# Kernel tuning notes

Measured on AMD Instinct MI355X. Metric: run time of the kernel, lower is better.

## Reference

```python
import jax, jax.numpy as jnp
import numpy as np

VOCAB = 32000
EMB = 512
HID = 512
SEQ = 64
BSZ = 32
SENTS = 48


def setup_inputs() -> dict:
    key = jax.random.key(0)
    ks = jax.random.split(key, 8)
    N = BSZ * SENTS
    s = 1.0 / np.sqrt(HID)
    return {
        "concept": jax.random.randint(ks[0], (N, SEQ), 0, VOCAB, dtype=jnp.int32),
        "ex_segs": SENTS,
        "emb_table": jax.random.normal(ks[1], (VOCAB, EMB), jnp.float32) * 0.02,
        "W_eh": jax.random.normal(ks[2], (HID, EMB), jnp.float32) * (1.0 / np.sqrt(EMB)),
        "b_eh": jnp.zeros((HID,), jnp.float32),
        "h0": jax.random.normal(ks[3], (1, HID), jnp.float32) * s,
        "W_in": jax.random.normal(ks[4], (HID, HID), jnp.float32) * s,
        "W_out": jax.random.normal(ks[5], (HID, 2 * HID), jnp.float32) * s,
        "W_ih": jax.random.normal(ks[6], (3 * HID, HID), jnp.float32) * s,
        "W_hh": jax.random.normal(ks[7], (3 * HID, HID), jnp.float32) * s,
        "b_ih": jnp.zeros((3 * HID,), jnp.float32),
        "b_hh": jnp.zeros((3 * HID,), jnp.float32),
    }


def reference(concept, ex_segs, emb_table, W_eh, b_eh, h0, W_in, W_out, W_ih, W_hh, b_ih, b_hh):
    N, S = concept.shape
    bsz = N // ex_segs
    H = W_eh.shape[0]
    # embedding lookup + emb_2_hid (dropout is identity in eval)
    emb = emb_table[concept]                              # [N, S, E]
    lengths = jnp.maximum((concept != 0).sum(-1), 1)      # [N], min 1 like pad value
    hid = jax.nn.elu(jnp.einsum('nse,he->nsh', emb, W_eh) + b_eh)  # [N, S, H]
    # uniform ex_segs: pad_sequence == reshape
    mem = hid.reshape(bsz, ex_segs, S, H).transpose(1, 0, 2, 3)    # [sent, b, S, H]
    lens = lengths.reshape(bsz, ex_segs).T                          # [sent, b]
    pos = jnp.arange(S)

    def step(h, xs):
        m, l = xs                                   # m: [b,S,H], l: [b]
        # GlobalAttention('general'): score = (h W_in) . m
        q = h @ W_in.T
        scores = jnp.einsum('bd,bsd->bs', q, m)
        scores = jnp.where(pos[None, :] < l[:, None], scores, -jnp.inf)
        align = jax.nn.softmax(scores, axis=-1)
        c = jnp.einsum('bs,bsd->bd', align, m)
        x = jnp.tanh(jnp.concatenate([c, h], axis=-1) @ W_out.T)
        # GRUCell
        gi = x @ W_ih.T + b_ih
        gh = h @ W_hh.T + b_hh
        ir, iz, inn = jnp.split(gi, 3, axis=-1)
        hr, hz, hn = jnp.split(gh, 3, axis=-1)
        r = jax.nn.sigmoid(ir + hr)
        z = jax.nn.sigmoid(iz + hz)
        n = jnp.tanh(inn + r * hn)
        h_new = (1.0 - z) * n + z * h
        return h_new, None

    h_init = jnp.broadcast_to(h0, (bsz, H))
    h_final, _ = jax.lax.scan(step, h_init, (mem, lens))
    # uniform segments: one-hot(ex_segs-1) gather == last step's hidden state
    return h_final
```

## Files before the change

kernel.cpp:

```cpp
#include <hip/hip_runtime.h>
#include <hip/hip_bf16.h>
#include <stdint.h>


typedef __bf16 bf16_t;
typedef __bf16 bf16x8 __attribute__((ext_vector_type(8)));
typedef float  f32x4  __attribute__((ext_vector_type(4)));
typedef unsigned u32x4 __attribute__((ext_vector_type(4)));

#define MFMA16(a,b,c) __builtin_amdgcn_mfma_f32_16x16x32_bf16((a),(b),(c),0,0,0)

static constexpr int    RW     = 12;
static constexpr size_t V_RING = 0;
static constexpr size_t V_WEH  = V_RING + (size_t)RW*32*65536*2;
static constexpr size_t V_W2   = V_WEH + 524288;
static constexpr size_t V_WH   = V_W2  + 1048576;
static constexpr size_t V_WI   = V_WH  + 2097152;
static constexpr size_t V_LEN  = V_WI  + 1572864;
static constexpr size_t V_H    = V_LEN + 8192;
static constexpr size_t V_HBF  = V_H   + 65536;
static constexpr size_t V_GH   = V_HBF + 32768;
static constexpr size_t V_HW2  = V_GH  + 196608;
static constexpr size_t V_XC   = V_HW2 + 65536;
static constexpr size_t V_FLG  = V_XC  + 65536;
static constexpr size_t V_REL  = V_FLG + 4096;
static constexpr size_t V_PD   = V_REL + 64;
static constexpr size_t WS_V4  = V_PD  + 6144;

static constexpr size_t L_MEM   = 0;
static constexpr size_t L_WA    = 100663296;
static constexpr size_t L_WOUT  = L_WA + 2097152;
static constexpr size_t L_WIH   = L_WOUT + 1048576;
static constexpr size_t L_LEN   = L_WIH + 1572864;
static constexpr size_t L_H     = L_LEN + 8192;
static constexpr size_t L_HBF   = L_H + 65536;
static constexpr size_t L_Q     = L_HBF + 32768;
static constexpr size_t L_GH    = L_Q + 65536;
static constexpr size_t L_CBF   = L_GH + 196608;
static constexpr size_t L_XBF   = L_CBF + 32768;
static constexpr size_t L_BAR   = L_XBF + 32768;
static constexpr size_t WS_LEG  = L_BAR + 256;

__device__ __forceinline__ unsigned ld_a32(const void* p) {
  return __hip_atomic_load((const unsigned*)p, __ATOMIC_RELAXED, __HIP_MEMORY_SCOPE_AGENT);
}
__device__ __forceinline__ unsigned long long ld_a64(const void* p) {
  return __hip_atomic_load((const unsigned long long*)p, __ATOMIC_RELAXED, __HIP_MEMORY_SCOPE_AGENT);
}
__device__ __forceinline__ void st_a32(void* p, unsigned v) {
  __hip_atomic_store((unsigned*)p, v, __ATOMIC_RELAXED, __HIP_MEMORY_SCOPE_AGENT);
}
__device__ __forceinline__ void st_a64(void* p, unsigned long long v) {
  __hip_atomic_store((unsigned long long*)p, v, __ATOMIC_RELAXED, __HIP_MEMORY_SCOPE_AGENT);
}
__device__ __forceinline__ void ld16u(u32x4& d, const void* p) {
  asm volatile("global_load_dwordx4 %0, %1, off sc0 sc1"
               : "=v"(d) : "v"(p) : "memory");
}
__device__ __forceinline__ void ld16f(f32x4& d, const void* p) {
  asm volatile("global_load_dwordx4 %0, %1, off sc0 sc1"
               : "=v"(d) : "v"(p) : "memory");
}
__device__ __forceinline__ void st16(void* p, f32x4 d) {
  asm volatile("global_store_dwordx4 %0, %1, off sc0 sc1"
               :: "v"(p), "v"(d) : "memory");
}
__device__ __forceinline__ void vm_wait0() {
  asm volatile("s_waitcnt vmcnt(0)" ::: "memory");
  __builtin_amdgcn_sched_barrier(0);
}
__device__ __forceinline__ void vm_wait16() {
  asm volatile("s_waitcnt vmcnt(16)" ::: "memory");
  __builtin_amdgcn_sched_barrier(0);
}
__device__ __forceinline__ float lo_f(unsigned long long u) {
  return __builtin_bit_cast(float, (unsigned)(u & 0xffffffffu));
}
__device__ __forceinline__ float hi_f(unsigned long long u) {
  return __builtin_bit_cast(float, (unsigned)(u >> 32));
}
__device__ __forceinline__ unsigned long long pack_f2(float a, float b) {
  return (unsigned long long)__builtin_bit_cast(unsigned, a)
       | ((unsigned long long)__builtin_bit_cast(unsigned, b) << 32);
}
__device__ __forceinline__ float2 bf2f(unsigned u) {
  float2 r;
  unsigned lo = u << 16, hi = u & 0xffff0000u;
  r.x = __builtin_bit_cast(float, lo);
  r.y = __builtin_bit_cast(float, hi);
  return r;
}
__device__ __forceinline__ unsigned pack_bf2(float a, float b) {
  __bf16 ba = (__bf16)a, bb = (__bf16)b;
  unsigned short ua = __builtin_bit_cast(unsigned short, ba);
  unsigned short ub = __builtin_bit_cast(unsigned short, bb);
  return (unsigned)ua | ((unsigned)ub << 16);
}
__device__ __forceinline__ bf16x8 cvt8(float4 lo, float4 hi) {
  bf16x8 v;
  v[0]=(__bf16)lo.x; v[1]=(__bf16)lo.y; v[2]=(__bf16)lo.z; v[3]=(__bf16)lo.w;
  v[4]=(__bf16)hi.x; v[5]=(__bf16)hi.y; v[6]=(__bf16)hi.z; v[7]=(__bf16)hi.w;
  return v;
}
__device__ __forceinline__ float fsig(float x) {
  return __builtin_amdgcn_rcpf(1.f + __expf(-x));
}
__device__ __forceinline__ float ftanh(float x) {
  float e = __expf(-2.f * fabsf(x));
  float t = (1.f - e) * __builtin_amdgcn_rcpf(1.f + e);
  return __builtin_copysignf(t, x);
}
__device__ __forceinline__ void gbar(unsigned* cnt, int target) {
  __syncthreads();
  if (threadIdx.x == 0) {
    __hip_atomic_fetch_add(cnt, 1u, __ATOMIC_RELAXED, __HIP_MEMORY_SCOPE_AGENT);
    while ((int)__hip_atomic_load(cnt, __ATOMIC_RELAXED, __HIP_MEMORY_SCOPE_AGENT) < target) {
      __builtin_amdgcn_s_sleep(1);
    }
  }
  __syncthreads();
}
__device__ __forceinline__ void cbar(unsigned* flags, unsigned* rel, int myb, int phase) {
  vm_wait0();
  __syncthreads();
  if (threadIdx.x < 64) {
    if (threadIdx.x == 0)
      st_a32(flags + myb, (unsigned)phase);
    const unsigned* fp = flags + threadIdx.x;
    for (;;) {
      int v = (int)ld_a32(fp);
      if (__all(v >= phase)) break;
      __builtin_amdgcn_s_sleep(2);
    }
    if (myb == 0 && threadIdx.x == 0)
      st_a32(rel, (unsigned)phase);
  }
  __syncthreads();
}

#define LDS_AT(base, row, kb) ((base) + (size_t)(row)*1024 + ((kb) ^ (((row) & 7) << 4)))

__global__ __launch_bounds__(256) void h_init(
    const float* __restrict__ h0, float* __restrict__ h, bf16_t* __restrict__ hbf)
{
  int idx = blockIdx.x * 256 + threadIdx.x;
  float v = h0[idx & 511];
  h[idx] = v;
  hbf[idx] = (__bf16)v;
}

__global__ __launch_bounds__(256) void lengths_kernel(
    const int* __restrict__ cpt, int* __restrict__ len)
{
  int r = blockIdx.x * 256 + threadIdx.x;
  if (r < 1536) {
    int c = 0;
    for (int s = 0; s < 64; ++s) c += (cpt[r*64 + s] != 0);
    len[r] = c > 1 ? c : 1;
  }
}

__global__ __launch_bounds__(256) void prep_v4(
    const float* __restrict__ Weh, const float* __restrict__ Win,
    const float* __restrict__ Wout, const float* __restrict__ Whh,
    const float* __restrict__ Wih,
    bf16_t* __restrict__ WehB, bf16_t* __restrict__ W2,
    bf16_t* __restrict__ WH, bf16_t* __restrict__ WI)
{
  int idx = blockIdx.x * 256 + threadIdx.x;
  if (idx < 262144) {
    WehB[idx] = (__bf16)Weh[idx];
  } else if (idx < 786432) {
    int t = idx - 262144;
    int r = t >> 9, d = t & 511;
    float v = (r < 512) ? Win[(size_t)d*512 + r] : Wout[(size_t)(r-512)*1024 + d];
    W2[t] = (__bf16)v;
  } else if (idx < 1835008) {
    int t = idx - 786432;
    int r = t >> 9, d = t & 511;
    float v = (r < 1536) ? Whh[(size_t)r*512 + d] : Wout[(size_t)(r-1536)*1024 + 512 + d];
    WH[t] = (__bf16)v;
  } else if (idx < 2621440) {
    int t = idx - 1835008;
    WI[t] = (__bf16)Wih[t];
  }
}

__global__ __launch_bounds__(256, 1) void fused_scan(
    const int* __restrict__ cpt, const float* __restrict__ table,
    const float* __restrict__ beh, const int* __restrict__ lengths,
    const bf16_t* __restrict__ WehB, const bf16_t* __restrict__ W2,
    const bf16_t* __restrict__ WH, const bf16_t* __restrict__ WI,
    const float* __restrict__ b_ih, const float* __restrict__ b_hh,
    const float* __restrict__ h0,
    bf16_t* __restrict__ ring,
    float* __restrict__ ght, float* __restrict__ hW2t, float* __restrict__ xct,
    float* __restrict__ h, bf16_t* __restrict__ hbf,
    unsigned* __restrict__ flags, unsigned* __restrict__ rel,
    unsigned* __restrict__ pd, float* __restrict__ out)
{
  __shared__ __align__(16) unsigned char smem[131072];

  const int tid = threadIdx.x, lane = tid & 63, w = tid >> 6;
  const int quad = lane >> 4, l15 = lane & 15;

  if (blockIdx.x >= 64) {
    unsigned char* A1 = smem;
    unsigned char* ME = smem + 65536;
    const int pid = blockIdx.x - 64;
    for (int c = pid; c < 1536; c += 192) {
      const int i = c >> 5, g = c & 31;
      if (i >= RW) {
        const int need = 2*(i - RW) + 1;
        if (tid == 0) {
          while ((int)ld_a32(rel) < need) __builtin_amdgcn_s_sleep(4);
        }
        __syncthreads();
      }
      {
        const int nrow = g*48 + i;
        const int s = tid >> 2, q = tid & 3;
        const int tok = cpt[nrow*64 + s];
        const float* tr = table + (size_t)tok*512 + q*128;
        #pragma unroll
        for (int it = 0; it < 16; ++it) {
          float4 lo = *(const float4*)(tr + it*8);
          float4 hi = *(const float4*)(tr + it*8 + 4);
          const int kb = q*256 + it*16;
          *(bf16x8*)LDS_AT(A1, s, kb) = cvt8(lo, hi);
        }
      }
      __syncthreads();
      for (int nb = 0; nb < 8; ++nb) {
        const int n0 = w*128 + nb*16;
        const bf16_t* brow = WehB + (size_t)(n0 + l15)*512;
        f32x4 ac0={0,0,0,0}, ac1={0,0,0,0}, ac2={0,0,0,0}, ac3={0,0,0,0};
        #pragma unroll
        for (int kt = 0; kt < 16; ++kt) {
          const int k = kt*32 + quad*8, k2 = k*2;
          bf16x8 bfr = *(const bf16x8*)(brow + k);
          bf16x8 x0 = *(const bf16x8*)LDS_AT(A1, l15,      k2);
          bf16x8 x1 = *(const bf16x8*)LDS_AT(A1, 16 + l15, k2);
          bf16x8 x2 = *(const bf16x8*)LDS_AT(A1, 32 + l15, k2);
          bf16x8 x3 = *(const bf16x8*)LDS_AT(A1, 48 + l15, k2);
          ac0 = MFMA16(x0, bfr, ac0);
          ac1 = MFMA16(x1, bfr, ac1);
          ac2 = MFMA16(x2, bfr, ac2);
          ac3 = MFMA16(x3, bfr, ac3);
        }
        const float bias = beh[n0 + l15];
        f32x4 av[4] = {ac0, ac1, ac2, ac3};
        #pragma unroll
        for (int mt = 0; mt < 4; ++mt) {
          #pragma unroll
          for (int r = 0; r < 4; ++r) {
            const int m = mt*16 + quad*4 + r;
            float v = av[mt][r] + bias;
            v = v > 0.f ? v : expm1f(v);
            float v2 = __shfl_xor(v, 1);
            if ((l15 & 1) == 0) {
              const int kb = (n0 + l15)*2;
              *(unsigned*)LDS_AT(ME, m, kb) = pack_bf2(v, v2);
            }
          }
        }
      }
      __syncthreads();
      {
        bf16_t* rc = ring + ((size_t)((i % RW)*32 + g))*65536;
        for (int nb = 0; nb < 16; ++nb) {
          const int n0 = w*256 + nb*16;
          const bf16_t* brow = W2 + (size_t)(n0 + l15)*512;
          f32x4 ac0={0,0,0,0}, ac1={0,0,0,0}, ac2={0,0,0,0}, ac3={0,0,0,0};
          #pragma unroll
          for (int kt = 0; kt < 16; ++kt) {
            const int k = kt*32 + quad*8, k2 = k*2;
            bf16x8 bfr = *(const bf16x8*)(brow + k);
            bf16x8 x0 = *(const bf16x8*)LDS_AT(ME, l15,      k2);
            bf16x8 x1 = *(const bf16x8*)LDS_AT(ME, 16 + l15, k2);
            bf16x8 x2 = *(const bf16x8*)LDS_AT(ME, 32 + l15, k2);
            bf16x8 x3 = *(const bf16x8*)LDS_AT(ME, 48 + l15, k2);
            ac0 = MFMA16(x0, bfr, ac0);
            ac1 = MFMA16(x1, bfr, ac1);
            ac2 = MFMA16(x2, bfr, ac2);
            ac3 = MFMA16(x3, bfr, ac3);
          }
          f32x4 av[4] = {ac0, ac1, ac2, ac3};
          if (w < 2) {
            #pragma unroll
            for (int mt = 0; mt < 4; ++mt) {
              #pragma unroll
              for (int r = 0; r < 4; ++r) {
                const int m = mt*16 + quad*4 + r;
                float v = av[mt][r];
                float v2 = __shfl_xor(v, 1);
                if ((l15 & 1) == 0)
                  st_a32(rc + (size_t)m*512 + n0 + l15, pack_bf2(v, v2));
              }
            }
          } else {
            const int d = n0 + l15 - 512;
            #pragma unroll
            for (int mt = 0; mt < 4; ++mt) {
              #pragma unroll
              for (int r = 0; r < 4; r += 2) {
                const int m0 = mt*16 + quad*4 + r;
                st_a32(rc + 32768 + (size_t)d*64 + m0,
                       pack_bf2(av[mt][r], av[mt][r+1]));
              }
            }
          }
        }
      }
      __syncthreads();
      if (tid == 0)
        __hip_atomic_store(pd + c, 1u, __ATOMIC_RELEASE, __HIP_MEMORY_SCOPE_AGENT);
    }
    return;
  }

  unsigned short* x_lds = (unsigned short*)smem;
  float* hsm    = (float*)(smem + 16640);
  float* sc_lds = (float*)(smem + 18688);
  float* al_lds = (float*)(smem + 18944);
  float* gi_lds = (float*)(smem + 19200);

  const int g = blockIdx.x;
  const int p2 = g >> 3, q2 = g & 7;
  const int b_loc = tid >> 6, dl = tid & 63;
  const int bg = 4*p2 + b_loc, Dg = 64*q2 + dl;
  float hreg = h0[Dg];
  int phase = 0;

  for (int i = 0; i < 48; ++i) {
    if (g < 32) {
      if (tid == 0) {
        while (ld_a32(pd + (i*32 + g)) == 0u) __builtin_amdgcn_s_sleep(2);
      }
      { int t2 = tid * 2;
        unsigned long long v = ld_a64(h + g*512 + t2);
        hsm[t2] = lo_f(v); hsm[t2+1] = hi_f(v); }
      __syncthreads();
      const char* ringc = (const char*)(ring + ((size_t)((i % RW)*32 + g))*65536);
      const int s = tid >> 2, p = tid & 3;
      u32x4 pb[16], qb[16];
      {
        const char* pbase = ringc + s*1024 + p*256;
        #pragma unroll
        for (int it = 0; it < 16; ++it) ld16u(pb[it], pbase + it*16);
        const char* qbase = ringc + 65536 + (size_t)(tid*2)*128;
        #pragma unroll
        for (int it = 0; it < 16; ++it) ld16u(qb[it], qbase + it*16);
      }
      vm_wait16();
      {
        const float* qp = hsm + p*128;
        float sum = 0.f;
        #pragma unroll
        for (int it = 0; it < 16; ++it) {
          u32x4 u = pb[it];
          float2 f0 = bf2f(u[0]), f1 = bf2f(u[1]), f2 = bf2f(u[2]), f3 = bf2f(u[3]);
          const float* qq = qp + it*8;
          sum += f0.x*qq[0] + f0.y*qq[1] + f1.x*qq[2] + f1.y*qq[3]
               + f2.x*qq[4] + f2.y*qq[5] + f3.x*qq[6] + f3.y*qq[7];
        }
        sum += __shfl_xor(sum, 1);
        sum += __shfl_xor(sum, 2);
        if (p == 0) {
          int len = lengths[g*48 + i];
          sc_lds[s] = (s < len) ? sum : -1e30f;
        }
      }
      __syncthreads();
      if (tid < 64) {
        float v = sc_lds[tid];
        float mx = v;
        #pragma unroll
        for (int o = 32; o; o >>= 1) mx = fmaxf(mx, __shfl_xor(mx, o));
        float e = __expf(v - mx);
        float sm = e;
        #pragma unroll
        for (int o = 32; o; o >>= 1) sm += __shfl_xor(sm, o);
        al_lds[tid] = e * __builtin_amdgcn_rcpf(sm);
      }
      __syncthreads();
      vm_wait0();
      {
        const int d0 = tid * 2;
        float c0 = 0.f, c1 = 0.f;
        #pragma unroll
        for (int it = 0; it < 8; ++it) {
          u32x4 u = qb[it];
          const int s0 = it*8;
          float2 a0 = bf2f(u[0]), a1 = bf2f(u[1]), a2 = bf2f(u[2]), a3 = bf2f(u[3]);
          c0 += al_lds[s0]*a0.x + al_lds[s0+1]*a0.y + al_lds[s0+2]*a1.x + al_lds[s0+3]*a1.y
              + al_lds[s0+4]*a2.x + al_lds[s0+5]*a2.y + al_lds[s0+6]*a3.x + al_lds[s0+7]*a3.y;
        }
        #pragma unroll
        for (int it = 0; it < 8; ++it) {
          u32x4 u = qb[8+it];
          const int s0 = it*8;
          float2 a0 = bf2f(u[0]), a1 = bf2f(u[1]), a2 = bf2f(u[2]), a3 = bf2f(u[3]);
          c1 += al_lds[s0]*a0.x + al_lds[s0+1]*a0.y + al_lds[s0+2]*a1.x + al_lds[s0+3]*a1.y
              + al_lds[s0+4]*a2.x + al_lds[s0+5]*a2.y + al_lds[s0+6]*a3.x + al_lds[s0+7]*a3.y;
        }
        st_a32(xct + (size_t)d0*32 + g,     __builtin_bit_cast(unsigned, c0));
        st_a32(xct + (size_t)(d0+1)*32 + g, __builtin_bit_cast(unsigned, c1));
      }
    } else {
      const int q3 = g - 32, pg = q3 >> 3, qg = q3 & 7;
      const int R0 = 256*qg;
      {
        const int r = tid >> 5, c32 = tid & 31;
        const char* src = (const char*)(hbf + (size_t)(8*pg + r)*512) + c32*32;
        u32x4 a, b2;
        ld16u(a, src); ld16u(b2, src + 16);
        vm_wait0();
        char* dst = (char*)x_lds + r*1040 + c32*32;
        *(u32x4*)dst = a; *(u32x4*)(dst + 16) = b2;
      }
      __syncthreads();
      f32x4 acc[4];
      #pragma unroll
      for (int t = 0; t < 4; ++t) acc[t] = (f32x4){0,0,0,0};
      const int Rw = R0 + 64*w;
      #pragma unroll
      for (int kt = 0; kt < 16; ++kt) {
        const int k = kt*32 + quad*8;
        bf16x8 a0 = *(const bf16x8*)((char*)x_lds + l15*1040 + k*2);
        #pragma unroll
        for (int nt = 0; nt < 4; ++nt) {
          bf16x8 bfr = *(const bf16x8*)(WH + (size_t)(Rw + nt*16 + l15)*512 + k);
          acc[nt] = MFMA16(a0, bfr, acc[nt]);
        }
      }
      if (quad < 2) {
        #pragma unroll
        for (int nt = 0; nt < 4; ++nt) {
          const int R = Rw + nt*16 + l15;
          if (R < 1536) {
            const float bias = b_hh[R];
            f32x4 vals = {acc[nt][0]+bias, acc[nt][1]+bias, acc[nt][2]+bias, acc[nt][3]+bias};
            st16(ght + (size_t)R*32 + 8*pg + quad*4, vals);
          } else {
            st16(hW2t + (size_t)(R - 1536)*32 + 8*pg + quad*4, acc[nt]);
          }
        }
      }
    }
    cbar(flags, rel, g, ++phase);

    {
      const int c = tid * 2;
      f32x4 xa, xb2, ha, hb2;
      ld16f(xa,  xct  + (size_t)c*32 + 4*p2);
      ld16f(ha,  hW2t + (size_t)c*32 + 4*p2);
      ld16f(xb2, xct  + (size_t)(c+1)*32 + 4*p2);
      ld16f(hb2, hW2t + (size_t)(c+1)*32 + 4*p2);
      vm_wait0();
      #pragma unroll
      for (int r = 0; r < 4; ++r) {
        float x0 = ftanh(xa[r] + ha[r]);
        float x1 = ftanh(xb2[r] + hb2[r]);
        *(unsigned*)((char*)x_lds + r*1040 + c*2) = pack_bf2(x0, x1);
      }
    }
    __syncthreads();
    {
      const bf16_t* wp[3];
      #pragma unroll
      for (int nt = 0; nt < 3; ++nt) {
        const int lr = w*48 + nt*16 + l15;
        wp[nt] = WI + ((size_t)((lr >> 6)*512 + 64*q2 + (lr & 63)))*512;
      }
      f32x4 ga[3];
      #pragma unroll
      for (int t = 0; t < 3; ++t) ga[t] = (f32x4){0,0,0,0};
      #pragma unroll
      for (int kt = 0; kt < 16; ++kt) {
        const int k = kt*32 + quad*8;
        bf16x8 a0 = *(const bf16x8*)((char*)x_lds + l15*1040 + k*2);
        #pragma unroll
        for (int nt = 0; nt < 3; ++nt) {
          bf16x8 bfr = *(const bf16x8*)(wp[nt] + k);
          ga[nt] = MFMA16(a0, bfr, ga[nt]);
        }
      }
      if (quad == 0) {
        #pragma unroll
        for (int nt = 0; nt < 3; ++nt) {
          const int lr = w*48 + nt*16 + l15;
          #pragma unroll
          for (int r = 0; r < 4; ++r) gi_lds[lr*4 + r] = ga[nt][r];
        }
      }
    }
    __syncthreads();
    {
      float ir = gi_lds[dl*4 + b_loc]        + b_ih[Dg];
      float iz = gi_lds[(64+dl)*4 + b_loc]   + b_ih[512 + Dg];
      float in = gi_lds[(128+dl)*4 + b_loc]  + b_ih[1024 + Dg];
      float hr = __builtin_bit_cast(float, ld_a32(ght + (size_t)Dg*32 + bg));
      float hz = __builtin_bit_cast(float, ld_a32(ght + (size_t)(512 + Dg)*32 + bg));
      float hn = __builtin_bit_cast(float, ld_a32(ght + (size_t)(1024 + Dg)*32 + bg));
      float rr = fsig(ir + hr);
      float zz = fsig(iz + hz);
      float nn = ftanh(in + rr * hn);
      float res = (1.f - zz) * nn + zz * hreg;
      hreg = res;
      if (i == 47) {
        out[bg*512 + Dg] = res;
      } else {
        float o2 = __shfl_xor(res, 1);
        if ((dl & 1) == 0) {
          st_a64(h + bg*512 + Dg, pack_f2(res, o2));
          st_a32(hbf + bg*512 + Dg, pack_bf2(res, o2));
        }
      }
    }
    if (i == 47) break;
    cbar(flags, rel, g, ++phase);
  }
}

__global__ __launch_bounds__(256) void prep_legacy(
    const float* __restrict__ Win, const float* __restrict__ Whh,
    const float* __restrict__ Wout, const float* __restrict__ Wih,
    bf16_t* __restrict__ WA, bf16_t* __restrict__ WoutB, bf16_t* __restrict__ WihB)
{
  int idx = blockIdx.x * 256 + threadIdx.x;
  if (idx < 262144)        WA[idx]            = (__bf16)Win[idx];
  else if (idx < 1048576)  WA[idx]            = (__bf16)Whh[idx - 262144];
  else if (idx < 1572864)  WoutB[idx-1048576] = (__bf16)Wout[idx - 1048576];
  else if (idx < 2359296)  WihB[idx-1572864]  = (__bf16)Wih[idx - 1572864];
}

__global__ __launch_bounds__(256) void embed_gemm(
    const int* __restrict__ cpt, const float* __restrict__ table,
    const float* __restrict__ Weh, const float* __restrict__ beh,
    bf16_t* __restrict__ mem)
{
  __shared__ unsigned short A_lds[64][40];
  __shared__ unsigned short B_lds[64][40];
  const int bid = blockIdx.x;
  const int M0 = (bid >> 3) * 64;
  const int N0 = (bid & 7) * 64;
  const int tid = threadIdx.x, lane = tid & 63, w = tid >> 6;
  const int l15 = lane & 15, quad = lane >> 4;
  const int srow = tid >> 2;
  const int koff = (tid & 3) * 8;
  const int tok = cpt[M0 + srow];
  const float* arow = table + (size_t)tok * 512;
  const float* brow = Weh + (size_t)(N0 + srow) * 512;

  f32x4 acc0 = {0,0,0,0}, acc1 = {0,0,0,0}, acc2 = {0,0,0,0}, acc3 = {0,0,0,0};
  for (int kt = 0; kt < 16; ++kt) {
    const int k0 = kt * 32;
    float4 alo = *(const float4*)(arow + k0 + koff);
    float4 ahi = *(const float4*)(arow + k0 + koff + 4);
    float4 blo = *(const float4*)(brow + k0 + koff);
    float4 bhi = *(const float4*)(brow + k0 + koff + 4);
    __syncthreads();
    *(bf16x8*)(&A_lds[srow][koff]) = cvt8(alo, ahi);
    *(bf16x8*)(&B_lds[srow][koff]) = cvt8(blo, bhi);
    __syncthreads();
    const int kq = quad * 8;
    bf16x8 bfr = *(const bf16x8*)(&B_lds[16*w + l15][kq]);
    bf16x8 a0 = *(const bf16x8*)(&A_lds[l15][kq]);
    bf16x8 a1 = *(const bf16x8*)(&A_lds[16 + l15][kq]);
    bf16x8 a2 = *(const bf16x8*)(&A_lds[32 + l15][kq]);
    bf16x8 a3 = *(const bf16x8*)(&A_lds[48 + l15][kq]);
    acc0 = MFMA16(a0, bfr, acc0);
    acc1 = MFMA16(a1, bfr, acc1);
    acc2 = MFMA16(a2, bfr, acc2);
    acc3 = MFMA16(a3, bfr, acc3);
  }
  const int n = N0 + 16*w + l15;
  const float bias = beh[n];
  f32x4 accs[4] = {acc0, acc1, acc2, acc3};
  #pragma unroll
  for (int mt = 0; mt < 4; ++mt) {
    #pragma unroll
    for (int r = 0; r < 4; ++r) {
      int m = M0 + mt*16 + quad*4 + r;
      float v = accs[mt][r] + bias;
      v = v > 0.f ? v : expm1f(v);
      int s = m & 63, nrow = m >> 6;
      int sent = nrow % 48, b = nrow / 48;
      mem[(((size_t)(sent*32 + b))*64 + s)*512 + n] = (__bf16)v;
    }
  }
}

__global__ __launch_bounds__(256) void scan_legacy(
    const bf16_t* __restrict__ mem, const int* __restrict__ lengths,
    const bf16_t* __restrict__ WA, const bf16_t* __restrict__ Wout, const bf16_t* __restrict__ Wih,
    const float* __restrict__ b_ih, const float* __restrict__ b_hh,
    float* __restrict__ q, float* __restrict__ gh,
    float* __restrict__ h, bf16_t* __restrict__ hbf,
    bf16_t* __restrict__ cbf, bf16_t* __restrict__ xbf,
    unsigned* __restrict__ bar, float* __restrict__ out)
{
  __shared__ __align__(16) unsigned char smem[52352];
  unsigned short* h_lds = (unsigned short*)smem;
  unsigned short* x_lds = (unsigned short*)smem;
  float* q_lds  = (float*)(smem + 33280);
  float* sc_lds = (float*)(smem + 35328);
  float* al_lds = (float*)(smem + 35584);
  unsigned short* c_lds = (unsigned short*)(smem + 33280);
  float* xb_lds = (float*)(smem + 50176);
  float* gi_lds = (float*)(smem + 33280);

  const int g = blockIdx.x, tid = threadIdx.x, lane = tid & 63, w = tid >> 6;
  const int quad = lane >> 4, l15 = lane & 15;
  int phase = 0;

  for (int i = 0; i < 48; ++i) {
    for (int it = 0; it < 16; ++it) {
      int chunk = tid + 256*it;
      int row = chunk >> 7, cc = chunk & 127;
      unsigned long long v = ld_a64(hbf + row*512 + cc*4);
      *(unsigned long long*)((char*)h_lds + row*1040 + cc*8) = v;
    }
    __syncthreads();
    {
      f32x4 acc0 = {0,0,0,0}, acc1 = {0,0,0,0};
      const int nrow = 64*g + 16*w + l15;
      const bf16_t* wrow = WA + (size_t)nrow * 512;
      #pragma unroll
      for (int kt = 0; kt < 16; ++kt) {
        const int k = kt*32 + quad*8;
        bf16x8 bfr = *(const bf16x8*)(wrow + k);
        bf16x8 a0 = *(const bf16x8*)((char*)h_lds + l15*1040 + k*2);
        bf16x8 a1 = *(const bf16x8*)((char*)h_lds + (16 + l15)*1040 + k*2);
        acc0 = MFMA16(a0, bfr, acc0);
        acc1 = MFMA16(a1, bfr, acc1);
      }
      const float bias = (nrow >= 512) ? b_hh[nrow - 512] : 0.f;
      #pragma unroll
      for (int r = 0; r < 4; ++r) {
        int b0 = quad*4 + r;
        float v0 = acc0[r] + bias, v1 = acc1[r] + bias;
        if (nrow < 512) {
          st_a32(q + b0*512 + nrow,        __builtin_bit_cast(unsigned, v0));
          st_a32(q + (b0+16)*512 + nrow,   __builtin_bit_cast(unsigned, v1));
        } else {
          st_a32(gh + b0*1536 + nrow-512,      __builtin_bit_cast(unsigned, v0));
          st_a32(gh + (b0+16)*1536 + nrow-512, __builtin_bit_cast(unsigned, v1));
        }
      }
    }
    gbar(bar, ++phase * 32);
    {
      for (int it = 0; it < 2; ++it) {
        int idx = tid + 256*it;
        unsigned v = ld_a32(q + g*512 + idx);
        q_lds[idx] = __builtin_bit_cast(float, v);
      }
      __syncthreads();
      const bf16_t* mrow = mem + ((size_t)(i*32 + g)) * 64 * 512;
      {
        const int s = tid >> 2, p = tid & 3;
        const uint4* mp = (const uint4*)(mrow + s*512 + p*128);
        const float* qp = q_lds + p*128;
        float sum = 0.f;
        #pragma unroll
        for (int it = 0; it < 16; ++it) {
          uint4 u = mp[it];
          float2 f0 = bf2f(u.x), f1 = bf2f(u.y), f2 = bf2f(u.z), f3 = bf2f(u.w);
          const float* qq = qp + it*8;
          sum += f0.x*qq[0] + f0.y*qq[1] + f1.x*qq[2] + f1.y*qq[3]
               + f2.x*qq[4] + f2.y*qq[5] + f3.x*qq[6] + f3.y*qq[7];
        }
        sum += __shfl_xor(sum, 1);
        sum += __shfl_xor(sum, 2);
        if (p == 0) {
          int len = lengths[g*48 + i];
          sc_lds[s] = (s < len) ? sum : -1e30f;
        }
      }
      __syncthreads();
      if (tid < 64) {
        float v = sc_lds[tid];
        float mx = v;
        #pragma unroll
        for (int o = 32; o; o >>= 1) mx = fmaxf(mx, __shfl_xor(mx, o));
        float e = __expf(v - mx);
        float sm = e;
        #pragma unroll
        for (int o = 32; o; o >>= 1) sm += __shfl_xor(sm, o);
        al_lds[tid] = e / sm;
      }
      __syncthreads();
      {
        const int d0 = tid * 2;
        float c0 = 0.f, c1 = 0.f;
        for (int s2 = 0; s2 < 64; ++s2) {
          unsigned u = *(const unsigned*)(mrow + s2*512 + d0);
          float2 f = bf2f(u);
          float a = al_lds[s2];
          c0 += a * f.x; c1 += a * f.y;
        }
        st_a32(cbf + g*512 + d0, pack_bf2(c0, c1));
      }
    }
    gbar(bar, ++phase * 32);
    {
      f32x4 acc = {0,0,0,0};
      const int nrow = 16*g + l15;
      const bf16_t* wrow = Wout + (size_t)nrow * 1024;
      for (int kh = 0; kh < 2; ++kh) {
        for (int it = 0; it < 8; ++it) {
          int cid = tid + 256*it;
          int row = cid >> 6, cc = cid & 63;
          unsigned long long v = ld_a64(cbf + row*512 + kh*256 + cc*4);
          *(unsigned long long*)((char*)c_lds + row*528 + cc*8) = v;
        }
        __syncthreads();
        if (w < 2) {
          #pragma unroll
          for (int kt = 0; kt < 8; ++kt) {
            const int kl = kt*32 + quad*8;
            bf16x8 bfr = *(const bf16x8*)(wrow + kh*256 + kl);
            bf16x8 af  = *(const bf16x8*)((char*)c_lds + (16*w + l15)*528 + kl*2);
            acc = MFMA16(af, bfr, acc);
          }
        }
        __syncthreads();
      }
      if (w < 2) {
        #pragma unroll
        for (int kt = 0; kt < 16; ++kt) {
          const int k = kt*32 + quad*8;
          bf16x8 bfr = *(const bf16x8*)(wrow + 512 + k);
          bf16x8 af  = *(const bf16x8*)((char*)h_lds + (16*w + l15)*1040 + k*2);
          acc = MFMA16(af, bfr, acc);
        }
        #pragma unroll
        for (int r = 0; r < 4; ++r)
          xb_lds[w*272 + l15*17 + quad*4 + r] = acc[r];
      }
      __syncthreads();
      {
        const int b = tid >> 3, np = tid & 7;
        const int mt = b >> 4, ml = b & 15;
        float v0 = ftanh(xb_lds[mt*272 + (2*np)*17 + ml]);
        float v1 = ftanh(xb_lds[mt*272 + (2*np+1)*17 + ml]);
        st_a32(xbf + b*512 + 16*g + 2*np, pack_bf2(v0, v1));
      }
    }
    gbar(bar, ++phase * 32);
    {
      for (int it = 0; it < 16; ++it) {
        int chunk = tid + 256*it;
        int row = chunk >> 7, cc = chunk & 127;
        unsigned long long v = ld_a64(xbf + row*512 + cc*4);
        *(unsigned long long*)((char*)x_lds + row*1040 + cc*8) = v;
      }
      __syncthreads();
      #pragma unroll
      for (int tt = 0; tt < 2; ++tt) {
        const int t = w + 4*tt;
        if (t < 6) {
          const int nt = t % 3, mt = t / 3;
          f32x4 acc = {0,0,0,0};
          const int nrow = nt*512 + 16*g + l15;
          const bf16_t* wrow = Wih + (size_t)nrow * 512;
          #pragma unroll
          for (int kt = 0; kt < 16; ++kt) {
            const int k = kt*32 + quad*8;
            bf16x8 bfr = *(const bf16x8*)(wrow + k);
            bf16x8 af  = *(const bf16x8*)((char*)x_lds + (16*mt + l15)*1040 + k*2);
            acc = MFMA16(af, bfr, acc);
          }
          #pragma unroll
          for (int r = 0; r < 4; ++r)
            gi_lds[t*272 + l15*17 + quad*4 + r] = acc[r];
        }
      }
      __syncthreads();
      {
        const int b = tid >> 3, dlp = tid & 7;
        const int mt = b >> 4, ml = b & 15;
        const int d0 = 16*g + 2*dlp;
        unsigned long long ur = ld_a64(gh + b*1536 + d0);
        unsigned long long uz = ld_a64(gh + b*1536 + 512 + d0);
        unsigned long long un = ld_a64(gh + b*1536 + 1024 + d0);
        unsigned long long uh = ld_a64(h + b*512 + d0);
        float res[2];
        #pragma unroll
        for (int e = 0; e < 2; ++e) {
          int dl = 2*dlp + e;
          float ir = gi_lds[(mt*3+0)*272 + dl*17 + ml] + b_ih[16*g + dl];
          float iz = gi_lds[(mt*3+1)*272 + dl*17 + ml] + b_ih[512 + 16*g + dl];
          float in = gi_lds[(mt*3+2)*272 + dl*17 + ml] + b_ih[1024 + 16*g + dl];
          float hr = e ? hi_f(ur) : lo_f(ur);
          float hz = e ? hi_f(uz) : lo_f(uz);
          float hn = e ? hi_f(un) : lo_f(un);
          float ho = e ? hi_f(uh) : lo_f(uh);
          float rr = fsig(ir + hr);
          float zz = fsig(iz + hz);
          float nn = ftanh(in + rr * hn);
          res[e] = (1.f - zz) * nn + zz * ho;
        }
        if (i == 47) {
          out[b*512 + d0]     = res[0];
          out[b*512 + d0 + 1] = res[1];
        } else {
          st_a64(h + b*512 + d0, pack_f2(res[0], res[1]));
          st_a32(hbf + b*512 + d0, pack_bf2(res[0], res[1]));
        }
      }
    }
    gbar(bar, ++phase * 32);
  }
}

extern "C" void kernel_launch(void* const* d_in, const int* in_sizes, int n_in,
                              void* d_out, int out_size, void* d_ws, size_t ws_size,
                              hipStream_t stream) {
  const int*   cpt   = (const int*)d_in[0];
  const float* table = (const float*)d_in[2];
  const float* Weh   = (const float*)d_in[3];
  const float* beh   = (const float*)d_in[4];
  const float* h0    = (const float*)d_in[5];
  const float* Win   = (const float*)d_in[6];
  const float* Wout  = (const float*)d_in[7];
  const float* Wih   = (const float*)d_in[8];
  const float* Whh   = (const float*)d_in[9];
  const float* bih   = (const float*)d_in[10];
  const float* bhh   = (const float*)d_in[11];
  char* ws = (char*)d_ws;

  if (ws_size >= WS_V4) {
    bf16_t* ring = (bf16_t*)(ws + V_RING);
    bf16_t* WehB = (bf16_t*)(ws + V_WEH);
    bf16_t* W2   = (bf16_t*)(ws + V_W2);
    bf16_t* WH   = (bf16_t*)(ws + V_WH);
    bf16_t* WI   = (bf16_t*)(ws + V_WI);
    int*    len  = (int*)(ws + V_LEN);
    float*  h    = (float*)(ws + V_H);
    bf16_t* hbf  = (bf16_t*)(ws + V_HBF);
    float*  ght  = (float*)(ws + V_GH);
    float*  hW2t = (float*)(ws + V_HW2);
    float*  xct  = (float*)(ws + V_XC);
    unsigned* flags = (unsigned*)(ws + V_FLG);
    unsigned* rel   = (unsigned*)(ws + V_REL);
    unsigned* pd    = (unsigned*)(ws + V_PD);

    hipMemsetAsync(ws + V_FLG, 0, 4096 + 64 + 6144, stream);
    prep_v4<<<10240, 256, 0, stream>>>(Weh, Win, Wout, Whh, Wih, WehB, W2, WH, WI);
    h_init<<<64, 256, 0, stream>>>(h0, h, hbf);
    lengths_kernel<<<6, 256, 0, stream>>>(cpt, len);
    fused_scan<<<256, 256, 0, stream>>>(cpt, table, beh, len,
                                        WehB, W2, WH, WI, bih, bhh, h0,
                                        ring, ght, hW2t, xct, h, hbf,
                                        flags, rel, pd, (float*)d_out);
  } else if (ws_size >= WS_LEG) {
    bf16_t* mem   = (bf16_t*)(ws + L_MEM);
    bf16_t* WA    = (bf16_t*)(ws + L_WA);
    bf16_t* WoutB = (bf16_t*)(ws + L_WOUT);
    bf16_t* WihB  = (bf16_t*)(ws + L_WIH);
    int*    len   = (int*)(ws + L_LEN);
    float*  h     = (float*)(ws + L_H);
    bf16_t* hbf   = (bf16_t*)(ws + L_HBF);
    float*  q     = (float*)(ws + L_Q);
    float*  gh    = (float*)(ws + L_GH);
    bf16_t* cbf   = (bf16_t*)(ws + L_CBF);
    bf16_t* xbf   = (bf16_t*)(ws + L_XBF);
    unsigned* bar = (unsigned*)(ws + L_BAR);

    hipMemsetAsync(bar, 0, 256, stream);
    prep_legacy<<<9216, 256, 0, stream>>>(Win, Whh, Wout, Wih, WA, WoutB, WihB);
    h_init<<<64, 256, 0, stream>>>(h0, h, hbf);
    lengths_kernel<<<6, 256, 0, stream>>>(cpt, len);
    embed_gemm<<<12288, 256, 0, stream>>>(cpt, table, Weh, beh, mem);
    scan_legacy<<<32, 256, 0, stream>>>(mem, len, WA, WoutB, WihB, bih, bhh,
                                        q, gh, h, hbf, cbf, xbf, bar, (float*)d_out);
  }
}
```

Before: 1.333 ms.

## Split attention across all 64 scan blocks with extra grid barrier

The attention step (scores, softmax, context) is spread over all 64 scan blocks instead of 32. Each batch row is now handled by two blocks that each cover half the sequence positions and half the hidden dims. Partial scores go through a global scratch buffer, and an added grid barrier sits between score computation and the softmax/context stage. This halves per-block load and ALU work on the serial critical path, at the cost of one more grid-wide barrier per step and updated producer release counts.

Measured after the change: 1.865 ms. 1.4x slower.

```diff
diff --git a/kernel.cpp b/kernel.cpp
--- a/kernel.cpp
+++ b/kernel.cpp
@@ -25,7 +25,8 @@
 static constexpr size_t V_FLG  = V_XC  + 65536;
 static constexpr size_t V_REL  = V_FLG + 4096;
 static constexpr size_t V_PD   = V_REL + 64;
-static constexpr size_t WS_V4  = V_PD  + 6144;
+static constexpr size_t V_SCX  = V_PD  + 6144;
+static constexpr size_t WS_V4  = V_SCX + 8192;
 
 static constexpr size_t L_MEM   = 0;
 static constexpr size_t L_WA    = 100663296;
@@ -69,8 +70,12 @@
   asm volatile("s_waitcnt vmcnt(0)" ::: "memory");
   __builtin_amdgcn_sched_barrier(0);
 }
-__device__ __forceinline__ void vm_wait16() {
-  asm volatile("s_waitcnt vmcnt(16)" ::: "memory");
+__device__ __forceinline__ void vm_wait8() {
+  asm volatile("s_waitcnt vmcnt(8)" ::: "memory");
+  __builtin_amdgcn_sched_barrier(0);
+}
+__device__ __forceinline__ void vm_wait10() {
+  asm volatile("s_waitcnt vmcnt(10)" ::: "memory");
   __builtin_amdgcn_sched_barrier(0);
 }
 __device__ __forceinline__ float lo_f(unsigned long long u) {
@@ -197,7 +202,8 @@
     float* __restrict__ ght, float* __restrict__ hW2t, float* __restrict__ xct,
     float* __restrict__ h, bf16_t* __restrict__ hbf,
     unsigned* __restrict__ flags, unsigned* __restrict__ rel,
-    unsigned* __restrict__ pd, float* __restrict__ out)
+    unsigned* __restrict__ pd, float* __restrict__ scex,
+    float* __restrict__ out)
 {
   __shared__ __align__(16) unsigned char smem[131072];
 
@@ -211,7 +217,7 @@
     for (int c = pid; c < 1536; c += 192) {
       const int i = c >> 5, g = c & 31;
       if (i >= RW) {
-        const int need = 2*(i - RW) + 1;
+        const int need = 3*(i - RW) + 2;
         if (tid == 0) {
           while ((int)ld_a32(rel) < need) __builtin_amdgcn_s_sleep(4);
         }
@@ -321,103 +327,74 @@
 
   unsigned short* x_lds = (unsigned short*)smem;
   float* hsm    = (float*)(smem + 16640);
-  float* sc_lds = (float*)(smem + 18688);
   float* al_lds = (float*)(smem + 18944);
   float* gi_lds = (float*)(smem + 19200);
 
-  const int g = blockIdx.x;
-  const int p2 = g >> 3, q2 = g & 7;
+  const int b = blockIdx.x;
+  const int g = b & 31, half = b >> 5;
+  const int p2 = b >> 3, q2 = b & 7;
   const int b_loc = tid >> 6, dl = tid & 63;
   const int bg = 4*p2 + b_loc, Dg = 64*q2 + dl;
+  const int srow = half*32 + (tid >> 3), sseg = tid & 7;
+  const int drow = half*256 + tid;
   float hreg = h0[Dg];
   int phase = 0;
 
   for (int i = 0; i < 48; ++i) {
-    if (g < 32) {
-      if (tid == 0) {
-        while (ld_a32(pd + (i*32 + g)) == 0u) __builtin_amdgcn_s_sleep(2);
-      }
-      { int t2 = tid * 2;
-        unsigned long long v = ld_a64(h + g*512 + t2);
-        hsm[t2] = lo_f(v); hsm[t2+1] = hi_f(v); }
-      __syncthreads();
-      const char* ringc = (const char*)(ring + ((size_t)((i % RW)*32 + g))*65536);
-      const int s = tid >> 2, p = tid & 3;
-      u32x4 pb[16], qb[16];
-      {
-        const char* pbase = ringc + s*1024 + p*256;
-        #pragma unroll
-        for (int it = 0; it < 16; ++it) ld16u(pb[it], pbase + it*16);
-        const char* qbase = ringc + 65536 + (size_t)(tid*2)*128;
-        #pragma unroll
-        for (int it = 0; it < 16; ++it) ld16u(qb[it], qbase + it*16);
-      }
-      vm_wait16();
-      {
-        const float* qp = hsm + p*128;
-        float sum = 0.f;
-        #pragma unroll
-        for (int it = 0; it < 16; ++it) {
-          u32x4 u = pb[it];
-          float2 f0 = bf2f(u[0]), f1 = bf2f(u[1]), f2 = bf2f(u[2]), f3 = bf2f(u[3]);
-          const float* qq = qp + it*8;
-          sum += f0.x*qq[0] + f0.y*qq[1] + f1.x*qq[2] + f1.y*qq[3]
-               + f2.x*qq[4] + f2.y*qq[5] + f3.x*qq[6] + f3.y*qq[7];
-        }
-        sum += __shfl_xor(sum, 1);
-        sum += __shfl_xor(sum, 2);
-        if (p == 0) {
-          int len = lengths[g*48 + i];
-          sc_lds[s] = (s < len) ? sum : -1e30f;
-        }
-      }
-      __syncthreads();
-      if (tid < 64) {
-        float v = sc_lds[tid];
-        float mx = v;
-        #pragma unroll
-        for (int o = 32; o; o >>= 1) mx = fmaxf(mx, __shfl_xor(mx, o));
-        float e = __expf(v - mx);
-        float sm = e;
-        #pragma unroll
-        for (int o = 32; o; o >>= 1) sm += __shfl_xor(sm, o);
-        al_lds[tid] = e * __builtin_amdgcn_rcpf(sm);
-      }
-      __syncthreads();
+    if (tid == 0) {
+      while (ld_a32(pd + (i*32 + g)) == 0u) __builtin_amdgcn_s_sleep(2);
+    }
+    { int t2 = tid * 2;
+      unsigned long long v = ld_a64(h + g*512 + t2);
+      hsm[t2] = lo_f(v); hsm[t2+1] = hi_f(v); }
+    __syncthreads();
+    const char* ringc = (const char*)(ring + ((size_t)((i % RW)*32 + g))*65536);
+    u32x4 pb[8], qb[8], hb0, hb1;
+    {
+      const char* pbase = ringc + (size_t)srow*1024 + sseg*128;
+      #pragma unroll
+      for (int j = 0; j < 8; ++j) ld16u(pb[j], pbase + j*16);
+      const char* qbase = ringc + 65536 + (size_t)drow*128;
+      #pragma unroll
+      for (int j = 0; j < 8; ++j) ld16u(qb[j], qbase + j*16);
+    }
+    if (b >= 32) {
+      const int q3 = b - 32, pg = q3 >> 3;
+      const int r = tid >> 5, c32 = tid & 31;
+      const char* src = (const char*)hbf + (size_t)(8*pg + r)*1024 + c32*32;
+      ld16u(hb0, src); ld16u(hb1, src + 16);
+      vm_wait10();
+    } else {
+      vm_wait8();
+    }
+    {
+      const float* qp = hsm + sseg*64;
+      float sum = 0.f;
+      #pragma unroll
+      for (int j = 0; j < 8; ++j) {
+        u32x4 u = pb[j];
+        float2 f0 = bf2f(u[0]), f1 = bf2f(u[1]), f2 = bf2f(u[2]), f3 = bf2f(u[3]);
+        const float* qq = qp + j*8;
+        sum += f0.x*qq[0] + f0.y*qq[1] + f1.x*qq[2] + f1.y*qq[3]
+             + f2.x*qq[4] + f2.y*qq[5] + f3.x*qq[6] + f3.y*qq[7];
+      }
+      sum += __shfl_xor(sum, 1);
+      sum += __shfl_xor(sum, 2);
+      sum += __shfl_xor(sum, 4);
+      if (sseg == 0) {
+        const int len = lengths[g*48 + i];
+        float sc = (srow < len) ? sum : -1e30f;
+        st_a32(scex + g*64 + srow, __builtin_bit_cast(unsigned, sc));
+      }
+    }
+    if (b >= 32) {
+      const int q3 = b - 32, pg = q3 >> 3, qg = q3 & 7;
+      const int R0 = 256*qg;
       vm_wait0();
       {
-        const int d0 = tid * 2;
-        float c0 = 0.f, c1 = 0.f;
-        #pragma unroll
-        for (int it = 0; it < 8; ++it) {
-          u32x4 u = qb[it];
-          const int s0 = it*8;
-          float2 a0 = bf2f(u[0]), a1 = bf2f(u[1]), a2 = bf2f(u[2]), a3 = bf2f(u[3]);
-          c0 += al_lds[s0]*a0.x + al_lds[s0+1]*a0.y + al_lds[s0+2]*a1.x + al_lds[s0+3]*a1.y
-              + al_lds[s0+4]*a2.x + al_lds[s0+5]*a2.y + al_lds[s0+6]*a3.x + al_lds[s0+7]*a3.y;
-        }
-        #pragma unroll
-        for (int it = 0; it < 8; ++it) {
-          u32x4 u = qb[8+it];
-          const int s0 = it*8;
-          float2 a0 = bf2f(u[0]), a1 = bf2f(u[1]), a2 = bf2f(u[2]), a3 = bf2f(u[3]);
-          c1 += al_lds[s0]*a0.x + al_lds[s0+1]*a0.y + al_lds[s0+2]*a1.x + al_lds[s0+3]*a1.y
-              + al_lds[s0+4]*a2.x + al_lds[s0+5]*a2.y + al_lds[s0+6]*a3.x + al_lds[s0+7]*a3.y;
-        }
-        st_a32(xct + (size_t)d0*32 + g,     __builtin_bit_cast(unsigned, c0));
-        st_a32(xct + (size_t)(d0+1)*32 + g, __builtin_bit_cast(unsigned, c1));
-      }
-    } else {
-      const int q3 = g - 32, pg = q3 >> 3, qg = q3 & 7;
-      const int R0 = 256*qg;
-      {
         const int r = tid >> 5, c32 = tid & 31;
-        const char* src = (const char*)(hbf + (size_t)(8*pg + r)*512) + c32*32;
-        u32x4 a, b2;
-        ld16u(a, src); ld16u(b2, src + 16);
-        vm_wait0();
         char* dst = (char*)x_lds + r*1040 + c32*32;
-        *(u32x4*)dst = a; *(u32x4*)(dst + 16) = b2;
+        *(u32x4*)dst = hb0; *(u32x4*)(dst + 16) = hb1;
       }
       __syncthreads();
       f32x4 acc[4];
@@ -448,7 +425,33 @@
         }
       }
     }
-    cbar(flags, rel, g, ++phase);
+    cbar(flags, rel, b, ++phase);
+
+    if (tid < 64) {
+      float v = __builtin_bit_cast(float, ld_a32(scex + g*64 + tid));
+      float mx = v;
+      #pragma unroll
+      for (int o = 32; o; o >>= 1) mx = fmaxf(mx, __shfl_xor(mx, o));
+      float e = __expf(v - mx);
+      float sm = e;
+      #pragma unroll
+      for (int o = 32; o; o >>= 1) sm += __shfl_xor(sm, o);
+      al_lds[tid] = e * __builtin_amdgcn_rcpf(sm);
+    }
+    __syncthreads();
+    {
+      float c0 = 0.f;
+      #pragma unroll
+      for (int j = 0; j < 8; ++j) {
+        u32x4 u = qb[j];
+        float2 a0 = bf2f(u[0]), a1 = bf2f(u[1]), a2 = bf2f(u[2]), a3 = bf2f(u[3]);
+        const float* ap = al_lds + j*8;
+        c0 += ap[0]*a0.x + ap[1]*a0.y + ap[2]*a1.x + ap[3]*a1.y
+            + ap[4]*a2.x + ap[5]*a2.y + ap[6]*a3.x + ap[7]*a3.y;
+      }
+      st_a32(xct + (size_t)drow*32 + g, __builtin_bit_cast(unsigned, c0));
+    }
+    cbar(flags, rel, b, ++phase);
 
     {
       const int c = tid * 2;
@@ -519,7 +522,7 @@
       }
     }
     if (i == 47) break;
-    cbar(flags, rel, g, ++phase);
+    cbar(flags, rel, b, ++phase);
   }
 }
 
@@ -847,6 +850,7 @@
     unsigned* flags = (unsigned*)(ws + V_FLG);
     unsigned* rel   = (unsigned*)(ws + V_REL);
     unsigned* pd    = (unsigned*)(ws + V_PD);
+    float*    scex  = (float*)(ws + V_SCX);
 
     hipMemsetAsync(ws + V_FLG, 0, 4096 + 64 + 6144, stream);
     prep_v4<<<10240, 256, 0, stream>>>(Weh, Win, Wout, Whh, Wih, WehB, W2, WH, WI);
@@ -855,7 +859,7 @@
     fused_scan<<<256, 256, 0, stream>>>(cpt, table, beh, len,
                                         WehB, W2, WH, WI, bih, bhh, h0,
                                         ring, ght, hW2t, xct, h, hbf,
-                                        flags, rel, pd, (float*)d_out);
+                                        flags, rel, pd, scex, (float*)d_out);
   } else if (ws_size >= WS_LEG) {
     bf16_t* mem   = (bf16_t*)(ws + L_MEM);
     bf16_t* WA    = (bf16_t*)(ws + L_WA);
```
